# Optimization experiments

Measured on AMD Instinct MI355X. Metric: run time of the kernel, lower is better.

Reference implementation:

```python
import jax, jax.numpy as jnp
import numpy as np

D_MODEL = 2048
D_HEAD = 128
N_HEADS = D_MODEL // D_HEAD
SEQ_LENS = (512, 768, 384, 384)  # packed varlen sequences, sum = 2048
L_TOTAL = sum(SEQ_LENS)
EPS = 1e-6


def setup_inputs() -> dict:
    key = jax.random.key(0)
    ks = jax.random.split(key, 8)
    x = jax.random.normal(ks[0], (L_TOTAL, D_MODEL), jnp.float32)
    # Flux-style rope table: pairwise-duplicated cos/sin, pe = concat([cos, sin], -1) -> (L, 2*d_head)
    half = D_HEAD // 2
    pos = np.arange(L_TOTAL, dtype=np.float32)[:, None]
    freqs = 1.0 / (10000.0 ** (np.arange(half, dtype=np.float32) / half))  # (half,)
    ang = pos * freqs[None, :]                      # (L, half)
    cos = np.repeat(np.cos(ang), 2, axis=-1)        # (L, d_head), duplicated per pair
    sin = np.repeat(np.sin(ang), 2, axis=-1)
    pe = jnp.asarray(np.concatenate([cos, sin], axis=-1))  # (L, 2*d_head)
    seq_lens = jnp.asarray(SEQ_LENS, dtype=jnp.int32)
    std = 0.02
    qkv_w = std * jax.random.truncated_normal(ks[1], -2.0, 2.0, (3 * D_MODEL, D_MODEL), jnp.float32)
    qkv_b = jnp.zeros((3 * D_MODEL,), jnp.float32)
    q_scale = jnp.ones((D_HEAD,), jnp.float32)
    k_scale = jnp.ones((D_HEAD,), jnp.float32)
    proj_w = std * jax.random.truncated_normal(ks[2], -2.0, 2.0, (D_MODEL, D_MODEL), jnp.float32)
    proj_b = jnp.zeros((D_MODEL,), jnp.float32)
    return {"x": x, "pe": pe, "seq_lens": seq_lens, "qkv_w": qkv_w, "qkv_b": qkv_b,
            "q_scale": q_scale, "k_scale": k_scale, "proj_w": proj_w, "proj_b": proj_b}


def _rms_norm(t, scale):
    tf = t.astype(jnp.float32)
    rrms = jax.lax.rsqrt(jnp.mean(tf * tf, axis=-1, keepdims=True) + EPS)
    return (tf * rrms * scale).astype(t.dtype)


def _apply_rope(t, pe):
    # t: (L, nh, dh); pe: (L, 2*dh) with pairwise-duplicated cos|sin
    L, nh, dh = t.shape
    c = pe[:, None, 0:dh:2]     # (L, 1, dh/2) per-pair cos
    s = pe[:, None, dh::2]      # (L, 1, dh/2) per-pair sin
    tr = t.reshape(L, nh, dh // 2, 2)
    t1, t2 = tr[..., 0], tr[..., 1]
    out = jnp.stack([t1 * c - t2 * s, t1 * s + t2 * c], axis=-1)
    return out.reshape(L, nh, dh)


def reference(x, pe, seq_lens, qkv_w, qkv_b, q_scale, k_scale, proj_w, proj_b):
    L = x.shape[0]
    qkv = x @ qkv_w.T + qkv_b                      # (L, 3*D)
    q, k, v = jnp.split(qkv, 3, axis=-1)
    q = q.reshape(L, N_HEADS, D_HEAD)
    k = k.reshape(L, N_HEADS, D_HEAD)
    v = v.reshape(L, N_HEADS, D_HEAD)
    q = _rms_norm(q, q_scale)
    k = _rms_norm(k, k_scale)
    q = _apply_rope(q, pe)
    k = _apply_rope(k, pe)
    # block-diagonal (packed varlen) attention
    n = seq_lens.shape[0]
    seg = jnp.repeat(jnp.arange(n, dtype=jnp.int32), seq_lens, total_repeat_length=L)  # (L,)
    mask = seg[:, None] == seg[None, :]            # (L, L) block-diagonal
    scale = 1.0 / jnp.sqrt(jnp.float32(D_HEAD))
    scores = jnp.einsum('lhd,mhd->hlm', q, k) * scale  # (nh, L, L)
    scores = jnp.where(mask[None], scores, jnp.finfo(scores.dtype).min)
    p = jax.nn.softmax(scores, axis=-1)
    out = jnp.einsum('hlm,mhd->lhd', p, v)         # (L, nh, dh)
    out = out.reshape(L, D_MODEL)
    return out @ proj_w.T + proj_b
```

## Files before the change

kernel.cpp:

```cpp
#include <hip/hip_runtime.h>

typedef unsigned short ushort_t;
typedef __attribute__((ext_vector_type(4))) float f4;
typedef __attribute__((ext_vector_type(8))) short s8v;
typedef __attribute__((ext_vector_type(8))) __bf16 bf8v;

#define AS1 __attribute__((address_space(1)))
#define AS3 __attribute__((address_space(3)))

__device__ __forceinline__ void async16(void* lds, const void* g) {
    __builtin_amdgcn_global_load_lds((AS1 const void*)g, (AS3 void*)lds, 16, 0, 0);
}

__device__ __forceinline__ f4 mfma16(s8v a, s8v b, f4 c) {
    return __builtin_amdgcn_mfma_f32_16x16x32_bf16(
        __builtin_bit_cast(bf8v, a), __builtin_bit_cast(bf8v, b), c, 0, 0, 0);
}

__device__ __forceinline__ ushort_t f2bf(float f) {
    unsigned int u = __float_as_uint(f);
    u += 0x7fffu + ((u >> 16) & 1u);
    return (ushort_t)(u >> 16);
}
__device__ __forceinline__ float bf2f(ushort_t u) {
    return __uint_as_float(((unsigned int)u) << 16);
}

#define L_TOT   2048
#define DMODEL  2048
#define DHEAD   128
#define NHEADS  16

__global__ __launch_bounds__(256) void cast_all(const float* __restrict__ x,
                                                const float* __restrict__ w1,
                                                const float* __restrict__ w2,
                                                ushort_t* __restrict__ xo,
                                                ushort_t* __restrict__ w1o,
                                                ushort_t* __restrict__ w2o) {
    int i = blockIdx.x * 256 + threadIdx.x;
    const float* src; ushort_t* dst; int off;
    if (i < 1048576)      { src = x;  dst = xo;  off = 0; }
    else if (i < 4194304) { src = w1; dst = w1o; off = 1048576; }
    else                  { src = w2; dst = w2o; off = 4194304; }
    int j = i - off;
    float4 v = ((const float4*)src)[j];
    ushort4 o;
    o.x = f2bf(v.x); o.y = f2bf(v.y); o.z = f2bf(v.z); o.w = f2bf(v.w);
    ((ushort4*)dst)[j] = o;
}


template <int P>
__device__ __forceinline__ void cluster(f4 (&acc)[8][4], const s8v (&af)[2][2],
                                        const s8v (&bf)[4][2]) {
    __builtin_amdgcn_s_setprio(1);
#pragma unroll
    for (int mm = 0; mm < 2; mm++)
#pragma unroll
        for (int nn = 0; nn < 4; nn++) {
            acc[2 * P + mm][nn] = mfma16(af[mm][0], bf[nn][0], acc[2 * P + mm][nn]);
            acc[2 * P + mm][nn] = mfma16(af[mm][1], bf[nn][1], acc[2 * P + mm][nn]);
        }
    __builtin_amdgcn_s_setprio(0);
}

#define LDF(base, row, oo) (*(const s8v*)&(base)[(row) * 64 + (oo)])

#define STG(dst, gb, Tt, h)                                                              \
    async16(&(dst)[tid * 8 + (2 * (h)) * 4096],                                          \
            (gb) + (size_t)(Tt) * 64 + (size_t)(128 * (h)) * K);                         \
    async16(&(dst)[tid * 8 + (2 * (h) + 1) * 4096],                                      \
            (gb) + (size_t)(Tt) * 64 + (size_t)(128 * (h) + 64) * K);

#define OPENB()                                                                          \
    __builtin_amdgcn_s_barrier();                                                        \
    asm volatile("s_waitcnt lgkmcnt(0)" ::: "memory");                                   \
    __builtin_amdgcn_sched_barrier(0);

#define TILE(cur, T)                                                                     \
    {                                                                                    \
        const int Tn1 = ((T) + 1 < NT) ? (T) + 1 : NT - 1;                               \
        const int Tn2 = ((T) + 2 < NT) ? (T) + 2 : NT - 1;                               \
        const ushort_t* fA = stA[cur];                                                   \
        const ushort_t* fB = stB[cur];                                                   \
        s8v bfrag[4][2];                                                                 \
        s8v afrag[2][2];                                                                 \
                                                                  \
        bfrag[0][0] = LDF(fB, brow + 0,  o0); bfrag[0][1] = LDF(fB, brow + 0,  o1);      \
        bfrag[1][0] = LDF(fB, brow + 16, o0); bfrag[1][1] = LDF(fB, brow + 16, o1);      \
        bfrag[2][0] = LDF(fB, brow + 32, o0); bfrag[2][1] = LDF(fB, brow + 32, o1);      \
        bfrag[3][0] = LDF(fB, brow + 48, o0); bfrag[3][1] = LDF(fB, brow + 48, o1);      \
        afrag[0][0] = LDF(fA, arow + 0,  o0); afrag[0][1] = LDF(fA, arow + 0,  o1);      \
        afrag[1][0] = LDF(fA, arow + 16, o0); afrag[1][1] = LDF(fA, arow + 16, o1);      \
        STG(stA[(cur) ^ 1], gA, Tn1, 0)                                                  \
        OPENB()                                                                          \
        cluster<0>(acc, afrag, bfrag);                                                   \
        __builtin_amdgcn_s_barrier();                                                    \
                                                                  \
        afrag[0][0] = LDF(fA, arow + 32, o0); afrag[0][1] = LDF(fA, arow + 32, o1);      \
        afrag[1][0] = LDF(fA, arow + 48, o0); afrag[1][1] = LDF(fA, arow + 48, o1);      \
        STG(stA[(cur) ^ 1], gA, Tn1, 1)                                                  \
        OPENB()                                                                          \
        cluster<1>(acc, afrag, bfrag);                                                   \
        __builtin_amdgcn_s_barrier();                                                    \
                                                                  \
        afrag[0][0] = LDF(fA, arow + 64, o0); afrag[0][1] = LDF(fA, arow + 64, o1);      \
        afrag[1][0] = LDF(fA, arow + 80, o0); afrag[1][1] = LDF(fA, arow + 80, o1);      \
        STG(stB[cur], gB, Tn2, 0)                                                        \
        OPENB()                                                                          \
        cluster<2>(acc, afrag, bfrag);                                                   \
        __builtin_amdgcn_s_barrier();                                                    \
                                                                  \
        afrag[0][0] = LDF(fA, arow + 96,  o0); afrag[0][1] = LDF(fA, arow + 96,  o1);    \
        afrag[1][0] = LDF(fA, arow + 112, o0); afrag[1][1] = LDF(fA, arow + 112, o1);    \
        STG(stB[cur], gB, Tn2, 1)                                                        \
        asm volatile("s_waitcnt vmcnt(4)" ::: "memory");                                 \
        __builtin_amdgcn_sched_barrier(0);                                               \
        OPENB()                                                                          \
        cluster<3>(acc, afrag, bfrag);                                                   \
        __builtin_amdgcn_s_barrier();                                                    \
    }

__global__ __launch_bounds__(512, 2) void gemm_qkv256(const ushort_t* __restrict__ A,
                                                      const ushort_t* __restrict__ Bt,
                                                      const float* __restrict__ bias,
                                                      ushort_t* __restrict__ qk_out,
                                                      ushort_t* __restrict__ vt_out,
                                                      int K) {
    __shared__ alignas(16) ushort_t sA[2][16384];
    __shared__ alignas(16) ushort_t sB[2][16384];

    const int tid  = threadIdx.x;
    const int lane = tid & 63;
    const int wave = tid >> 6;
    const int wm = wave >> 2;
    const int wn = wave & 3;

    const int phys = blockIdx.y * 8 + blockIdx.x;
    const int lid  = (phys & 7) * 24 + (phys >> 3);
    const int bxs  = lid & 7;
    const int bys  = lid >> 3;

    const int bm = bxs * 256;
    const int bn = bys * 256;
    const bool is_v = bys >= 16;
    const int NT = K >> 6;

    const int q15 = lane & 15;
    const int g   = lane >> 4;
    const int l7  = lane & 7;
    const int o0  = ((g    ) ^ l7) * 8;
    const int o1  = ((g + 4) ^ l7) * 8;
    const int arow = wm * 128 + q15;
    const int brow = wn * 64 + q15;

    const int rs  = tid >> 3;
    const int csw = ((tid & 7) ^ (rs & 7)) * 8;
    const ushort_t* Abase = A  + (size_t)(bm + rs) * K + csw;
    const ushort_t* Bbase = Bt + (size_t)(bn + rs) * K + csw;

    ushort_t* stA[2]; ushort_t* stB[2];
    const ushort_t* gA; const ushort_t* gB;
    if (!is_v) { stA[0] = sA[0]; stA[1] = sA[1]; stB[0] = sB[0]; stB[1] = sB[1];
                 gA = Abase; gB = Bbase; }
    else       { stA[0] = sB[0]; stA[1] = sB[1]; stB[0] = sA[0]; stB[1] = sA[1];
                 gA = Bbase; gB = Abase; }

    f4 acc[8][4];
#pragma unroll
    for (int i = 0; i < 8; i++)
#pragma unroll
        for (int j = 0; j < 4; j++) acc[i][j] = (f4){0.f, 0.f, 0.f, 0.f};

    STG(stA[0], gA, 0, 0) STG(stA[0], gA, 0, 1)
    STG(stB[0], gB, 0, 0) STG(stB[0], gB, 0, 1)
    {
        const int T1 = NT > 1 ? 1 : 0;
        STG(stB[1], gB, T1, 0) STG(stB[1], gB, T1, 1)
    }
    asm volatile("s_waitcnt vmcnt(4)" ::: "memory");
    __builtin_amdgcn_sched_barrier(0);
    __builtin_amdgcn_s_barrier();

    for (int T = 0; T < NT; T += 2) {
        TILE(0, T)
        TILE(1, T + 1)
    }

    if (!is_v) {
#pragma unroll
        for (int n = 0; n < 4; n++) {
            int col = bn + wn * 64 + n * 16 + q15;
            float bv = bias[col];
#pragma unroll
            for (int m = 0; m < 8; m++) {
                int r0 = bm + wm * 128 + m * 16 + g * 4;
#pragma unroll
                for (int r = 0; r < 4; r++)
                    qk_out[(size_t)(r0 + r) * 4096 + col] = f2bf(acc[m][n][r] + bv);
            }
        }
    } else {
        const int cb   = (bys - 16) * 256 + wm * 128;
        const int tok0 = bm + wn * 64 + q15;
#pragma unroll
        for (int m = 0; m < 8; m++) {
#pragma unroll
            for (int r = 0; r < 4; r++) {
                int c = cb + m * 16 + g * 4 + r;
                float bv = bias[4096 + c];
#pragma unroll
                for (int n = 0; n < 4; n++)
                    vt_out[(size_t)c * L_TOT + tok0 + n * 16] = f2bf(acc[m][n][r] + bv);
            }
        }
    }
}

__global__ __launch_bounds__(256) void gemm_proj(const ushort_t* __restrict__ A,
                                                 const ushort_t* __restrict__ Bt,
                                                 const float* __restrict__ bias,
                                                 float* __restrict__ out,
                                                 int K) {
    __shared__ alignas(16) ushort_t pA[128 * 64];
    __shared__ alignas(16) ushort_t pB[128 * 64];
    const int tid  = threadIdx.x;
    const int lane = tid & 63;
    const int wave = tid >> 6;
    const int wr = (wave >> 1) * 64;
    const int wc = (wave & 1) * 64;

    const int phys = blockIdx.y * 16 + blockIdx.x;
    const int lid  = (phys & 7) * 32 + (phys >> 3);
    const int bm = (lid & 15) * 128;
    const int bn = (lid >> 4) * 128;

    f4 acc[4][4];
#pragma unroll
    for (int i = 0; i < 4; i++)
#pragma unroll
        for (int j = 0; j < 4; j++) acc[i][j] = (f4){0.f, 0.f, 0.f, 0.f};

    const int rs  = tid >> 3;
    const int csw = ((tid & 7) ^ (rs & 7)) * 8;
    const ushort_t* Abase = A  + (size_t)(bm + rs) * K + csw;
    const ushort_t* Bbase = Bt + (size_t)(bn + rs) * K + csw;
    const int arow = wr + (lane & 15);
    const int brow = wc + (lane & 15);
    const int l7 = lane & 7;
    const int o0 = (((lane >> 4)    ) ^ l7) * 8;
    const int o1 = (((lane >> 4) + 4) ^ l7) * 8;

    for (int k0 = 0; k0 < K; k0 += 64) {
#pragma unroll
        for (int s = 0; s < 4; s++) {
            async16(&pA[tid * 8 + s * 2048], Abase + k0 + (size_t)(32 * s) * K);
            async16(&pB[tid * 8 + s * 2048], Bbase + k0 + (size_t)(32 * s) * K);
        }
        __syncthreads();

        s8v af[4], bfr[4];
#pragma unroll
        for (int i = 0; i < 4; i++) af[i]  = *(const s8v*)&pA[(arow + i * 16) * 64 + o0];
#pragma unroll
        for (int j = 0; j < 4; j++) bfr[j] = *(const s8v*)&pB[(brow + j * 16) * 64 + o0];
#pragma unroll
        for (int i = 0; i < 4; i++)
#pragma unroll
            for (int j = 0; j < 4; j++) acc[i][j] = mfma16(af[i], bfr[j], acc[i][j]);

#pragma unroll
        for (int i = 0; i < 4; i++) af[i]  = *(const s8v*)&pA[(arow + i * 16) * 64 + o1];
#pragma unroll
        for (int j = 0; j < 4; j++) bfr[j] = *(const s8v*)&pB[(brow + j * 16) * 64 + o1];
#pragma unroll
        for (int i = 0; i < 4; i++)
#pragma unroll
            for (int j = 0; j < 4; j++) acc[i][j] = mfma16(af[i], bfr[j], acc[i][j]);
        __syncthreads();
    }

    const int q = lane & 15;
    const int g = lane >> 4;
    const int crow0 = bm + wr + g * 4;
    const int ccol0 = bn + wc + q;
#pragma unroll
    for (int j = 0; j < 4; j++) {
        int col = ccol0 + j * 16;
        float bv = bias[col];
#pragma unroll
        for (int i = 0; i < 4; i++) {
#pragma unroll
            for (int r = 0; r < 4; r++)
                out[(size_t)(crow0 + i * 16 + r) * DMODEL + col] = acc[i][j][r] + bv;
        }
    }
}

__global__ __launch_bounds__(256) void norm_rope(const ushort_t* __restrict__ qk,
                                                 const float* __restrict__ pe,
                                                 const float* __restrict__ q_scale,
                                                 const float* __restrict__ k_scale,
                                                 ushort_t* __restrict__ qh,
                                                 ushort_t* __restrict__ kh) {
    int wid  = blockIdx.x * 4 + (threadIdx.x >> 6);
    int lane = threadIdx.x & 63;
    int l = wid >> 4;
    int h = wid & 15;

    const ushort_t* base = qk + (size_t)l * 4096 + h * DHEAD + 2 * lane;
    ushort2 qu = *(const ushort2*)base;
    ushort2 ku = *(const ushort2*)(base + 2048);
    float qvx = bf2f(qu.x), qvy = bf2f(qu.y);
    float kvx = bf2f(ku.x), kvy = bf2f(ku.y);

    float qss = qvx * qvx + qvy * qvy;
    float kss = kvx * kvx + kvy * kvy;
#pragma unroll
    for (int m = 32; m >= 1; m >>= 1) {
        qss += __shfl_xor(qss, m);
        kss += __shfl_xor(kss, m);
    }
    float qr = rsqrtf(qss * (1.0f / DHEAD) + 1e-6f);
    float kr = rsqrtf(kss * (1.0f / DHEAD) + 1e-6f);

    float c = pe[(size_t)l * 256 + 2 * lane];
    float s = pe[(size_t)l * 256 + 128 + 2 * lane];

    float q1 = qvx * qr * q_scale[2 * lane];
    float q2 = qvy * qr * q_scale[2 * lane + 1];
    float k1 = kvx * kr * k_scale[2 * lane];
    float k2 = kvy * kr * k_scale[2 * lane + 1];

    const float sc = 0.08838834764831845f;
    float qo0 = (q1 * c - q2 * s) * sc;
    float qo1 = (q1 * s + q2 * c) * sc;
    float ko0 = k1 * c - k2 * s;
    float ko1 = k1 * s + k2 * c;

    size_t o = ((size_t)h * L_TOT + l) * DHEAD + 2 * lane;
    ushort2 qp, kp;
    qp.x = f2bf(qo0); qp.y = f2bf(qo1);
    kp.x = f2bf(ko0); kp.y = f2bf(ko1);
    *(ushort2*)(qh + o) = qp;
    *(ushort2*)(kh + o) = kp;
}

__global__ __launch_bounds__(256) void attn_kernel(const ushort_t* __restrict__ qh,
                                                   const ushort_t* __restrict__ kh,
                                                   const ushort_t* __restrict__ vt,
                                                   ushort_t* __restrict__ attn_out) {
    __shared__ alignas(16) ushort_t sK[64 * 128];
    __shared__ alignas(16) ushort_t sV[128 * 64];
    __shared__ alignas(16) ushort_t sP[4][16 * 64];

    const int phys = blockIdx.y * 32 + blockIdx.x;
    const int lid  = (phys & 7) * 64 + (phys >> 3);
    const int qt = lid & 31;
    const int h  = lid >> 5;

    const int tid = threadIdx.x;
    const int lane = tid & 63;
    const int w = tid >> 6;
    const int qrow0 = qt * 64 + w * 16;

    int q0 = qt * 64;
    int seg_start, seg_end;
    if (q0 < 512)       { seg_start = 0;    seg_end = 512;  }
    else if (q0 < 1280) { seg_start = 512;  seg_end = 1280; }
    else if (q0 < 1664) { seg_start = 1280; seg_end = 1664; }
    else                { seg_start = 1664; seg_end = 2048; }

    const int g = lane >> 4;
    const int q = lane & 15;
    const int qa7 = q & 7;

    const ushort_t* ksrc[4];
    const ushort_t* vsrc[4];
#pragma unroll
    for (int i = 0; i < 4; i++) {
        int p = i * 256 + tid;
        ksrc[i] = kh + ((size_t)h * L_TOT + (p >> 4)) * DHEAD + ((p & 15) ^ ((p >> 4) & 7)) * 8;
        vsrc[i] = vt + ((size_t)h * DHEAD + (p >> 3)) * L_TOT + ((p & 7) ^ ((p >> 3) & 7)) * 8;
    }

    s8v qf[4];
    {
        const ushort_t* qbase = qh + ((size_t)h * L_TOT + qrow0 + q) * DHEAD;
#pragma unroll
        for (int kd = 0; kd < 4; kd++) qf[kd] = *(const s8v*)(qbase + kd * 32 + g * 8);
    }

    f4 o[8];
#pragma unroll
    for (int j = 0; j < 8; j++) o[j] = (f4){0.f, 0.f, 0.f, 0.f};
    float lsum[4] = {0.f, 0.f, 0.f, 0.f};

    for (int kt = seg_start; kt < seg_end; kt += 64) {
#pragma unroll
        for (int i = 0; i < 4; i++) {
            int p = i * 256 + tid;
            async16(&sK[p * 8], ksrc[i] + (size_t)kt * DHEAD);
            async16(&sV[p * 8], vsrc[i] + kt);
        }
        __syncthreads();

        f4 S[4];
#pragma unroll
        for (int tj = 0; tj < 4; tj++) {
            f4 st = (f4){0.f, 0.f, 0.f, 0.f};
#pragma unroll
            for (int kd = 0; kd < 4; kd++) {
                s8v bfrag = *(const s8v*)&sK[(tj * 16 + q) * 128 + (((kd * 4 + g) ^ qa7) * 8)];
                st = mfma16(qf[kd], bfrag, st);
            }
            S[tj] = st;
        }

#pragma unroll
        for (int tj = 0; tj < 4; tj++)
#pragma unroll
            for (int r = 0; r < 4; r++) {
                float p = __expf(S[tj][r]);
                S[tj][r] = p;
                lsum[r] += p;
            }

#pragma unroll
        for (int tj = 0; tj < 4; tj++) {
            int cg = tj * 2 + (q >> 3);
#pragma unroll
            for (int r = 0; r < 4; r++) {
                int prow = g * 4 + r;
                sP[w][prow * 64 + ((cg ^ (prow & 7)) * 8) + qa7] = f2bf(S[tj][r]);
            }
        }
        asm volatile("s_waitcnt lgkmcnt(0)" ::: "memory");

#pragma unroll
        for (int ks = 0; ks < 2; ks++) {
            s8v pf = *(const s8v*)&sP[w][q * 64 + (((ks * 4 + g) ^ qa7) * 8)];
#pragma unroll
            for (int j = 0; j < 8; j++) {
                s8v vf = *(const s8v*)&sV[(j * 16 + q) * 64 + (((ks * 4 + g) ^ qa7) * 8)];
                o[j] = mfma16(pf, vf, o[j]);
            }
        }
        __syncthreads();
    }

#pragma unroll
    for (int r = 0; r < 4; r++) {
        float rs = lsum[r];
        rs += __shfl_xor(rs, 1);
        rs += __shfl_xor(rs, 2);
        rs += __shfl_xor(rs, 4);
        rs += __shfl_xor(rs, 8);
        int row = qrow0 + g * 4 + r;
        float inv = 1.0f / rs;
#pragma unroll
        for (int j = 0; j < 8; j++) {
            attn_out[(size_t)row * DMODEL + h * DHEAD + j * 16 + q] = f2bf(o[j][r] * inv);
        }
    }
}

extern "C" void kernel_launch(void* const* d_in, const int* in_sizes, int n_in,
                              void* d_out, int out_size, void* d_ws, size_t ws_size,
                              hipStream_t stream) {
    const float* x       = (const float*)d_in[0];
    const float* pe      = (const float*)d_in[1];
    const float* qkv_w   = (const float*)d_in[3];
    const float* qkv_b   = (const float*)d_in[4];
    const float* q_scale = (const float*)d_in[5];
    const float* k_scale = (const float*)d_in[6];
    const float* proj_w  = (const float*)d_in[7];
    const float* proj_b  = (const float*)d_in[8];
    float* out = (float*)d_out;

    char* ws = (char*)d_ws;
    const size_t MB = 1024 * 1024;
    ushort_t* x_bf     = (ushort_t*)(ws + 0);
    ushort_t* wqkv_bf  = (ushort_t*)(ws + 8 * MB);
    ushort_t* wproj_bf = (ushort_t*)(ws + 32 * MB);
    ushort_t* qk_bf    = (ushort_t*)(ws + 40 * MB);
    ushort_t* qh       = (ushort_t*)(ws + 57 * MB);
    ushort_t* kh       = (ushort_t*)(ws + 65 * MB);
    ushort_t* vt       = (ushort_t*)(ws + 73 * MB);
    ushort_t* attn_b   = (ushort_t*)(ws + 81 * MB);

    cast_all<<<20480, 256, 0, stream>>>(x, qkv_w, proj_w, x_bf, wqkv_bf, wproj_bf);

    gemm_qkv256<<<dim3(8, 24), 512, 0, stream>>>(x_bf, wqkv_bf, qkv_b, qk_bf, vt, 2048);

    norm_rope<<<8192, 256, 0, stream>>>(qk_bf, pe, q_scale, k_scale, qh, kh);

    attn_kernel<<<dim3(32, 16), 256, 0, stream>>>(qh, kh, vt, attn_b);

    gemm_proj<<<dim3(16, 16), 256, 0, stream>>>(attn_b, wproj_bf, proj_b, out, 2048);
}
```

Before: 262.0 us.

## Double-buffer attention K/V, split-K projection GEMM, grid-stride cast kernel

The attention kernel now double-buffers K/V tiles in LDS, prefetching the next tile while computing the current one, and raises wave priority around its MFMA blocks. The projection GEMM is split along K into two halves across blockIdx.z, writing fp32 partials that a new reduce_bias kernel sums and adds bias to. This raises the number of proj blocks for better CU occupancy. The cast kernel becomes grid-stride with fewer blocks, and the block-index swizzle in gemm_proj is dropped. The trade-off is extra partial-buffer traffic plus one more kernel launch, and double-buffering doubles the K/V LDS footprint.

Measured after the change: 255.1 us. -2.6%, faster.

```diff
diff --git a/kernel.cpp b/kernel.cpp
--- a/kernel.cpp
+++ b/kernel.cpp
@@ -37,16 +37,17 @@
                                                 ushort_t* __restrict__ xo,
                                                 ushort_t* __restrict__ w1o,
                                                 ushort_t* __restrict__ w2o) {
-    int i = blockIdx.x * 256 + threadIdx.x;
-    const float* src; ushort_t* dst; int off;
-    if (i < 1048576)      { src = x;  dst = xo;  off = 0; }
-    else if (i < 4194304) { src = w1; dst = w1o; off = 1048576; }
-    else                  { src = w2; dst = w2o; off = 4194304; }
-    int j = i - off;
-    float4 v = ((const float4*)src)[j];
-    ushort4 o;
-    o.x = f2bf(v.x); o.y = f2bf(v.y); o.z = f2bf(v.z); o.w = f2bf(v.w);
-    ((ushort4*)dst)[j] = o;
+    for (int i = blockIdx.x * 256 + threadIdx.x; i < 5242880; i += 2048 * 256) {
+        const float* src; ushort_t* dst; int off;
+        if (i < 1048576)      { src = x;  dst = xo;  off = 0; }
+        else if (i < 4194304) { src = w1; dst = w1o; off = 1048576; }
+        else                  { src = w2; dst = w2o; off = 4194304; }
+        int j = i - off;
+        float4 v = ((const float4*)src)[j];
+        ushort4 o;
+        o.x = f2bf(v.x); o.y = f2bf(v.y); o.z = f2bf(v.z); o.w = f2bf(v.w);
+        ((ushort4*)dst)[j] = o;
+    }
 }
 
 
@@ -219,8 +220,7 @@
 
 __global__ __launch_bounds__(256) void gemm_proj(const ushort_t* __restrict__ A,
                                                  const ushort_t* __restrict__ Bt,
-                                                 const float* __restrict__ bias,
-                                                 float* __restrict__ out,
+                                                 float* __restrict__ Cf,
                                                  int K) {
     __shared__ alignas(16) ushort_t pA[128 * 64];
     __shared__ alignas(16) ushort_t pB[128 * 64];
@@ -229,11 +229,8 @@
     const int wave = tid >> 6;
     const int wr = (wave >> 1) * 64;
     const int wc = (wave & 1) * 64;
-
-    const int phys = blockIdx.y * 16 + blockIdx.x;
-    const int lid  = (phys & 7) * 32 + (phys >> 3);
-    const int bm = (lid & 15) * 128;
-    const int bn = (lid >> 4) * 128;
+    const int bm = blockIdx.x * 128;
+    const int bn = blockIdx.y * 128;
 
     f4 acc[4][4];
 #pragma unroll
@@ -250,8 +247,10 @@
     const int l7 = lane & 7;
     const int o0 = (((lane >> 4)    ) ^ l7) * 8;
     const int o1 = (((lane >> 4) + 4) ^ l7) * 8;
-
-    for (int k0 = 0; k0 < K; k0 += 64) {
+    const int kbeg = blockIdx.z * (K >> 1);
+    const int kend = kbeg + (K >> 1);
+
+    for (int k0 = kbeg; k0 < kend; k0 += 64) {
 #pragma unroll
         for (int s = 0; s < 4; s++) {
             async16(&pA[tid * 8 + s * 2048], Abase + k0 + (size_t)(32 * s) * K);
@@ -284,17 +283,27 @@
     const int g = lane >> 4;
     const int crow0 = bm + wr + g * 4;
     const int ccol0 = bn + wc + q;
+    float* Cp = Cf + (size_t)blockIdx.z * L_TOT * DMODEL;
 #pragma unroll
     for (int j = 0; j < 4; j++) {
         int col = ccol0 + j * 16;
-        float bv = bias[col];
 #pragma unroll
         for (int i = 0; i < 4; i++) {
 #pragma unroll
             for (int r = 0; r < 4; r++)
-                out[(size_t)(crow0 + i * 16 + r) * DMODEL + col] = acc[i][j][r] + bv;
-        }
-    }
+                Cp[(size_t)(crow0 + i * 16 + r) * DMODEL + col] = acc[i][j][r];
+        }
+    }
+}
+
+__global__ __launch_bounds__(256) void reduce_bias(const float* __restrict__ part,
+                                                   const float* __restrict__ bias,
+                                                   float* __restrict__ out) {
+    int i = blockIdx.x * 256 + threadIdx.x;
+    f4 a = ((const f4*)part)[i];
+    f4 b = ((const f4*)(part + (size_t)L_TOT * DMODEL))[i];
+    f4 bv = ((const f4*)bias)[i & 511];
+    ((f4*)out)[i] = a + b + bv;
 }
 
 __global__ __launch_bounds__(256) void norm_rope(const ushort_t* __restrict__ qk,
@@ -350,8 +359,8 @@
                                                    const ushort_t* __restrict__ kh,
                                                    const ushort_t* __restrict__ vt,
                                                    ushort_t* __restrict__ attn_out) {
-    __shared__ alignas(16) ushort_t sK[64 * 128];
-    __shared__ alignas(16) ushort_t sV[128 * 64];
+    __shared__ alignas(16) ushort_t sK[2][64 * 128];
+    __shared__ alignas(16) ushort_t sV[2][128 * 64];
     __shared__ alignas(16) ushort_t sP[4][16 * 64];
 
     const int phys = blockIdx.y * 32 + blockIdx.x;
@@ -396,26 +405,45 @@
     for (int j = 0; j < 8; j++) o[j] = (f4){0.f, 0.f, 0.f, 0.f};
     float lsum[4] = {0.f, 0.f, 0.f, 0.f};
 
+#pragma unroll
+    for (int i = 0; i < 4; i++) {
+        int p = i * 256 + tid;
+        async16(&sK[0][p * 8], ksrc[i] + (size_t)seg_start * DHEAD);
+        async16(&sV[0][p * 8], vsrc[i] + seg_start);
+    }
+
+    int cur = 0;
     for (int kt = seg_start; kt < seg_end; kt += 64) {
-#pragma unroll
-        for (int i = 0; i < 4; i++) {
-            int p = i * 256 + tid;
-            async16(&sK[p * 8], ksrc[i] + (size_t)kt * DHEAD);
-            async16(&sV[p * 8], vsrc[i] + kt);
-        }
+        if (kt + 64 < seg_end) {
+#pragma unroll
+            for (int i = 0; i < 4; i++) {
+                int p = i * 256 + tid;
+                async16(&sK[cur ^ 1][p * 8], ksrc[i] + (size_t)(kt + 64) * DHEAD);
+                async16(&sV[cur ^ 1][p * 8], vsrc[i] + (kt + 64));
+            }
+            asm volatile("s_waitcnt vmcnt(8)" ::: "memory");
+        } else {
+            asm volatile("s_waitcnt vmcnt(0)" ::: "memory");
+        }
+        __builtin_amdgcn_sched_barrier(0);
         __syncthreads();
 
+        const ushort_t* Kc = sK[cur];
+        const ushort_t* Vc = sV[cur];
+
         f4 S[4];
+        __builtin_amdgcn_s_setprio(1);
 #pragma unroll
         for (int tj = 0; tj < 4; tj++) {
             f4 st = (f4){0.f, 0.f, 0.f, 0.f};
 #pragma unroll
             for (int kd = 0; kd < 4; kd++) {
-                s8v bfrag = *(const s8v*)&sK[(tj * 16 + q) * 128 + (((kd * 4 + g) ^ qa7) * 8)];
+                s8v bfrag = *(const s8v*)&Kc[(tj * 16 + q) * 128 + (((kd * 4 + g) ^ qa7) * 8)];
                 st = mfma16(qf[kd], bfrag, st);
             }
             S[tj] = st;
         }
+        __builtin_amdgcn_s_setprio(0);
 
 #pragma unroll
         for (int tj = 0; tj < 4; tj++)
@@ -437,16 +465,19 @@
         }
         asm volatile("s_waitcnt lgkmcnt(0)" ::: "memory");
 
+        __builtin_amdgcn_s_setprio(1);
 #pragma unroll
         for (int ks = 0; ks < 2; ks++) {
             s8v pf = *(const s8v*)&sP[w][q * 64 + (((ks * 4 + g) ^ qa7) * 8)];
 #pragma unroll
             for (int j = 0; j < 8; j++) {
-                s8v vf = *(const s8v*)&sV[(j * 16 + q) * 64 + (((ks * 4 + g) ^ qa7) * 8)];
+                s8v vf = *(const s8v*)&Vc[(j * 16 + q) * 64 + (((ks * 4 + g) ^ qa7) * 8)];
                 o[j] = mfma16(pf, vf, o[j]);
             }
         }
+        __builtin_amdgcn_s_setprio(0);
         __syncthreads();
+        cur ^= 1;
     }
 
 #pragma unroll
@@ -488,8 +519,9 @@
     ushort_t* kh       = (ushort_t*)(ws + 65 * MB);
     ushort_t* vt       = (ushort_t*)(ws + 73 * MB);
     ushort_t* attn_b   = (ushort_t*)(ws + 81 * MB);
-
-    cast_all<<<20480, 256, 0, stream>>>(x, qkv_w, proj_w, x_bf, wqkv_bf, wproj_bf);
+    float*    part     = (float*)   (ws + 40 * MB);
+
+    cast_all<<<2048, 256, 0, stream>>>(x, qkv_w, proj_w, x_bf, wqkv_bf, wproj_bf);
 
     gemm_qkv256<<<dim3(8, 24), 512, 0, stream>>>(x_bf, wqkv_bf, qkv_b, qk_bf, vt, 2048);
 
@@ -497,5 +529,6 @@
 
     attn_kernel<<<dim3(32, 16), 256, 0, stream>>>(qh, kh, vt, attn_b);
 
-    gemm_proj<<<dim3(16, 16), 256, 0, stream>>>(attn_b, wproj_bf, proj_b, out, 2048);
-}
+    gemm_proj<<<dim3(16, 16, 2), 256, 0, stream>>>(attn_b, wproj_bf, part, 2048);
+    reduce_bias<<<4096, 256, 0, stream>>>(part, proj_b, out);
+}
```
